# Kernel optimization log

Hardware: AMD Instinct MI355X
Metric: run time of the kernel (lower is better)

Reference implementation:

```python
import jax, jax.numpy as jnp
import numpy as np

B, L, D = 4, 816, 2048
SEP = 768            # gemma (image+text) prefix length
P_LEN = 3            # proprio tokens inside the action-expert block
N, K, H = 8, 1, 256  # heads, kv heads (GQA), head dim
G = N // K
GEMMA_MLP, ACTION_MLP = 16384, 4096
SOFTCAP = 50.0
BIG_NEG = -2.3819763e38


def rms_norm(x, scale, eps=1e-6):
    var = jnp.mean(jnp.square(x.astype(jnp.float32)), axis=-1, keepdims=True)
    normed = x * jax.lax.rsqrt(var + eps)
    return (normed * (1.0 + scale)).astype(x.dtype)


def apply_rope(x, positions, max_wavelength=10_000):
    # x: [B, T, n, H], positions: [B, T]
    head_dim = x.shape[-1]
    freq_exp = (2.0 / head_dim) * jnp.arange(head_dim // 2, dtype=jnp.float32)
    timescale = max_wavelength ** freq_exp
    radians = positions[..., None].astype(jnp.float32) / timescale[None, None, :]
    radians = radians[..., None, :]  # [B, T, 1, H/2]
    sin, cos = jnp.sin(radians), jnp.cos(radians)
    x1, x2 = jnp.split(x, 2, axis=-1)
    return jnp.concatenate([x1 * cos - x2 * sin, x2 * cos + x1 * sin], axis=-1).astype(x.dtype)


def get_qkv(xn, positions, wq, wkv):
    # wq: [N, D, H], wkv: [2, K, D, H]
    q = jnp.einsum('btd,ndh->btnh', xn, wq)
    k = jnp.einsum('bsd,kdh->bskh', xn, wkv[0])
    v = jnp.einsum('bsd,kdh->bskh', xn, wkv[1])
    q = apply_rope(q, positions) * (H ** -0.5)  # query_pre_attn_norm='rsqrt_head_dim'
    k = apply_rope(k, positions)
    return q, k, v


def geglu_ffn(x, w_gating, w_linear):
    # gemma GeGLU: w_gating [2, D, hidden], w_linear [hidden, D]
    gate = jax.nn.gelu(jnp.einsum('btd,dh->bth', x, w_gating[0]))
    act = gate * jnp.einsum('btd,dh->bth', x, w_gating[1])
    return jnp.einsum('bth,hd->btd', act, w_linear)


def setup_inputs() -> dict:
    key = jax.random.key(0)
    ks = jax.random.split(key, 16)
    s = 0.02
    x = jax.random.normal(ks[0], (B, L, D), jnp.float32)
    positions = jnp.broadcast_to(jnp.arange(L, dtype=jnp.int32), (B, L))
    # PiZero block mask: full attention within gemma prefix; proprio and action
    # blocks attend to everything before them plus themselves (mask_ar cumsum trick).
    mask_ar = np.zeros(L, dtype=np.int64)
    mask_ar[SEP] = 1
    mask_ar[SEP + P_LEN] = 1
    cm = np.cumsum(mask_ar)
    attn = cm[None, :] <= cm[:, None]  # [L_q, L_kv]
    attn_mask = jnp.asarray(np.broadcast_to(attn[None, None], (B, 1, L, L)))
    return {
        'x': x,
        'positions': positions,
        'attn_mask': attn_mask,
        'separation_idx': SEP,
        'pre_attn_scale': jnp.zeros((D,), jnp.float32),
        'pre_ffw_scale': jnp.zeros((D,), jnp.float32),
        'gq_w': jax.random.normal(ks[1], (N, D, H), jnp.float32) * s,
        'gkv_w': jax.random.normal(ks[2], (2, K, D, H), jnp.float32) * s,
        'go_w': jax.random.normal(ks[3], (N, H, D), jnp.float32) * s,
        'aq_w': jax.random.normal(ks[4], (N, D, H), jnp.float32) * s,
        'akv_w': jax.random.normal(ks[5], (2, K, D, H), jnp.float32) * s,
        'ao_w': jax.random.normal(ks[6], (N, H, D), jnp.float32) * s,
        'g_gating': jax.random.normal(ks[7], (2, D, GEMMA_MLP), jnp.float32) * s,
        'g_linear': jax.random.normal(ks[8], (GEMMA_MLP, D), jnp.float32) * s,
        'a_gating': jax.random.normal(ks[9], (2, D, ACTION_MLP), jnp.float32) * s,
        'a_linear': jax.random.normal(ks[10], (ACTION_MLP, D), jnp.float32) * s,
    }


def reference(x, positions, attn_mask, separation_idx, pre_attn_scale, pre_ffw_scale,
              gq_w, gkv_w, go_w, aq_w, akv_w, ao_w,
              g_gating, g_linear, a_gating, a_linear):
    sep = separation_idx
    xg, xa = x[:, :sep, :], x[:, sep:, :]
    # shared pre-attention RMSNorm applied to both expert streams
    ng = rms_norm(xg, pre_attn_scale)
    na = rms_norm(xa, pre_attn_scale)
    pg, pa = positions[:, :sep], positions[:, sep:]
    qg, kg, vg = get_qkv(ng, pg, gq_w, gkv_w)
    qa, ka, va = get_qkv(na, pa, aq_w, akv_w)
    # joint attention over concatenated streams
    q = jnp.concatenate([qg, qa], axis=1)   # [B, L, N, H]
    k = jnp.concatenate([kg, ka], axis=1)   # [B, L, K, H]
    v = jnp.concatenate([vg, va], axis=1)
    Bq, T = q.shape[0], q.shape[1]
    qr = q.reshape(Bq, T, K, G, H)
    logits = jnp.einsum('btkgh,bskh->bkgts', qr, k)
    logits = jnp.tanh(logits / SOFTCAP) * SOFTCAP  # attn logit softcap
    logits = jnp.where(attn_mask[:, :, None, :, :], logits, BIG_NEG)
    probs = jax.nn.softmax(logits.astype(jnp.float32), axis=-1).astype(logits.dtype)
    attn_out = jnp.einsum('bkgts,bskh->btkgh', probs, v).reshape(Bq, T, N, H)
    # per-expert output projections
    og = jnp.einsum('btnh,nhd->btd', attn_out[:, :sep], go_w)
    oa = jnp.einsum('btnh,nhd->btd', attn_out[:, sep:], ao_w)

    def post(attn_o, res, gating, lin):
        # faithful to source: final residual is mlp(norm(attn+res)) + res
        h = rms_norm(attn_o + res, pre_ffw_scale)
        return geglu_ffn(h, gating, lin) + res

    yg = post(og, xg, g_gating, g_linear)
    ya = post(oa, xa, a_gating, a_linear)
    return jnp.concatenate([yg, ya], axis=1)
```

## Files before the change

### kernel.cpp

```cpp
#include <hip/hip_runtime.h>
#include <hip/hip_bf16.h>

typedef __bf16 bfx8 __attribute__((ext_vector_type(8)));
typedef __bf16 bfx4 __attribute__((ext_vector_type(4)));
typedef float f32x4 __attribute__((ext_vector_type(4)));

#define MFMA16(a, b, c) __builtin_amdgcn_mfma_f32_16x16x32_bf16((a), (b), (c), 0, 0, 0)

__device__ __forceinline__ void gl_lds16(const __bf16* g, __bf16* l) {
  __builtin_amdgcn_global_load_lds(
      (const __attribute__((address_space(1))) unsigned int*)(const void*)g,
      (__attribute__((address_space(3))) unsigned int*)(void*)l, 16, 0, 0);
}

__device__ __forceinline__ unsigned pack_bf2(float a, float b) {
  unsigned short ua = __builtin_bit_cast(unsigned short, (__bf16)a);
  unsigned short ub = __builtin_bit_cast(unsigned short, (__bf16)b);
  return (unsigned)ua | ((unsigned)ub << 16);
}

__device__ __forceinline__ float gelu_tanh_f(float x) {
  float u = 0.7978845608028654f * (x + 0.044715f * x * x * x);
  float t;
  if (u > 10.f) t = 1.f;
  else if (u < -10.f) t = -1.f;
  else { float e = __expf(2.f * u); t = (e - 1.f) / (e + 1.f); }
  return 0.5f * x * (1.f + t);
}

__global__ __launch_bounds__(256)
void rmsnorm_kernel(const float* __restrict__ X, const float* __restrict__ X2,
                    const float* __restrict__ scale, __bf16* __restrict__ out) {
  __shared__ float wsum[4];
  const int row = blockIdx.x, tid = threadIdx.x;
  const size_t base = (size_t)row * 2048;
  f32x4 v[2];
  float ss = 0.f;
#pragma unroll
  for (int i = 0; i < 2; ++i) {
    const int idx = tid * 4 + i * 1024;
    v[i] = *(const f32x4*)(X + base + idx);
    if (X2) { f32x4 u = *(const f32x4*)(X2 + base + idx); v[i] = v[i] + u; }
#pragma unroll
    for (int j = 0; j < 4; ++j) ss += v[i][j] * v[i][j];
  }
#pragma unroll
  for (int o = 32; o > 0; o >>= 1) ss += __shfl_xor(ss, o, 64);
  if ((tid & 63) == 0) wsum[tid >> 6] = ss;
  __syncthreads();
  const float tot = wsum[0] + wsum[1] + wsum[2] + wsum[3];
  const float rs = rsqrtf(tot * (1.f / 2048.f) + 1e-6f);
#pragma unroll
  for (int i = 0; i < 2; ++i) {
    const int idx = tid * 4 + i * 1024;
    f32x4 sc = *(const f32x4*)(scale + idx);
    bfx4 ov;
#pragma unroll
    for (int j = 0; j < 4; ++j) ov[j] = (__bf16)(v[i][j] * rs * (1.f + sc[j]));
    *(bfx4*)(out + base + idx) = ov;
  }
}

__global__ __launch_bounds__(256)
void rope_bf_kernel(__bf16* __restrict__ buf, const int* __restrict__ pos,
                    int nheads, int rstride, float outscale) {
  const int row = blockIdx.x;
  const float p = (float)pos[row];
  const int total = nheads * 128;
  const size_t rbase = (size_t)row * (size_t)rstride;
  for (int idx = threadIdx.x; idx < total; idx += 256) {
    const int n = idx >> 7, i = idx & 127;
    const float ts = __expf(-(float)i * 0.071955784f);
    float sn, cs;
    __sincosf(p * ts, &sn, &cs);
    __bf16* bp = buf + rbase + n * 256 + i;
    const float x1 = (float)bp[0], x2 = (float)bp[128];
    bp[0]   = (__bf16)((x1 * cs - x2 * sn) * outscale);
    bp[128] = (__bf16)((x2 * cs + x1 * sn) * outscale);
  }
}

__global__ __launch_bounds__(256)
void rope_kernel(const float* __restrict__ in, const int* __restrict__ pos,
                 __bf16* __restrict__ outp, int nheads, float outscale) {
  const int row = blockIdx.x;
  const float p = (float)pos[row];
  const int total = nheads * 128;
  const size_t rbase = (size_t)row * (size_t)(nheads * 256);
  for (int idx = threadIdx.x; idx < total; idx += 256) {
    const int n = idx >> 7, i = idx & 127;
    const float ts = __expf(-(float)i * 0.071955784f);
    float sn, cs;
    __sincosf(p * ts, &sn, &cs);
    const float* bp = in + rbase + n * 256 + i;
    const float x1 = bp[0], x2 = bp[128];
    __bf16* ob = outp + rbase + n * 256 + i;
    ob[0]   = (__bf16)((x1 * cs - x2 * sn) * outscale);
    ob[128] = (__bf16)((x2 * cs + x1 * sn) * outscale);
  }
}

__global__ __launch_bounds__(256)
void convw_kernel(const float* __restrict__ in, __bf16* __restrict__ out,
                  int K, int headDim) {
  __shared__ __bf16 tile[64][65];
  const int tc0 = blockIdx.x * 64;
  const int tk0 = blockIdx.y * 64;
  const int tid = threadIdx.x;
  const int cchunk = tid & 15, krow = tid >> 4;
  const int c = tc0 + cchunk * 4;
  const float* colbase = in + (size_t)(c / headDim) * (size_t)K * headDim + (c % headDim);
#pragma unroll
  for (int i = 0; i < 4; ++i) {
    const int k = tk0 + krow + i * 16;
    f32x4 v = *(const f32x4*)(colbase + (size_t)k * headDim);
#pragma unroll
    for (int j = 0; j < 4; ++j) tile[cchunk * 4 + j][krow + i * 16] = (__bf16)v[j];
  }
  __syncthreads();
  const int nks = K >> 5;
#pragma unroll
  for (int s = 0; s < 2; ++s) {
    const int ch = tid + s * 256;
    const int wc = ch >> 3, wk8 = (ch & 7) * 8;
    bfx8 v;
#pragma unroll
    for (int j = 0; j < 8; ++j) v[j] = tile[wc][wk8 + j];
    const int col = tc0 + wc;
    const int kchunk = (tk0 + wk8) >> 3;
    const int cp = col >> 7, m = col & 127;
    const int ks = kchunk >> 2, lg = kchunk & 3;
    const int p = lg ^ ((m >> 1) & 3);
    *(bfx8*)(out + ((size_t)(cp * nks + ks)) * 4096 + m * 32 + p * 8) = v;
  }
}

__global__ __launch_bounds__(256, 2)
void gemm_bt2(const __bf16* __restrict__ A, const __bf16* __restrict__ Bt,
              void* __restrict__ C, void* __restrict__ C2, const void* __restrict__ Extra,
              int Mpb, int lda, int strideA, int Kd,
              int ldc, int strideC, int mbPerBatch,
              int outMode, int ldct) {
  __shared__ __align__(16) __bf16 As[8192];
  __shared__ __align__(16) __bf16 Bs[8192];
  const int tid = threadIdx.x;
  const int lane = tid & 63;
  const int wid = tid >> 6;
  const int b = blockIdx.x / mbPerBatch;
  const int row0 = (blockIdx.x % mbPerBatch) * 128;
  const int col0 = blockIdx.y * 128;
  const __bf16* Ab = A + (size_t)b * strideA;
  const size_t nks = (size_t)(Kd >> 5);
  const __bf16* Bpan0 = Bt + ((size_t)(col0 >> 7)) * nks * 4096;
  const int wm = (wid >> 1) * 64, wn = (wid & 1) * 64;
  const int qi = lane & 15, g = lane >> 4;

  const int m0 = tid >> 2, p0 = tid & 3;
  const int lg0 = p0 ^ ((m0 >> 1) & 3);
  const int m1 = m0 + 64;
  const int lg1 = p0 ^ ((m1 >> 1) & 3);
  int mr0 = row0 + m0; if (mr0 >= Mpb) mr0 = Mpb - 1;
  int mr1 = row0 + m1; if (mr1 >= Mpb) mr1 = Mpb - 1;
  const __bf16* asrc0 = Ab + (size_t)mr0 * lda + lg0 * 8;
  const __bf16* asrc1 = Ab + (size_t)mr1 * lda + lg1 * 8;

  f32x4 acc[4][4];
#pragma unroll
  for (int i = 0; i < 4; ++i)
#pragma unroll
    for (int j = 0; j < 4; ++j) acc[i][j] = f32x4{0.f, 0.f, 0.f, 0.f};

  for (int k0 = 0; k0 < Kd; k0 += 64) {
    __syncthreads();
    gl_lds16(asrc0 + k0, &As[tid * 8]);
    gl_lds16(asrc1 + k0, &As[(tid + 256) * 8]);
    gl_lds16(asrc0 + k0 + 32, &As[4096 + tid * 8]);
    gl_lds16(asrc1 + k0 + 32, &As[4096 + (tid + 256) * 8]);
    const __bf16* pb = Bpan0 + (size_t)(k0 >> 5) * 4096;
    gl_lds16(pb + tid * 8, &Bs[tid * 8]);
    gl_lds16(pb + (tid + 256) * 8, &Bs[(tid + 256) * 8]);
    gl_lds16(pb + 4096 + tid * 8, &Bs[4096 + tid * 8]);
    gl_lds16(pb + 4096 + (tid + 256) * 8, &Bs[4096 + (tid + 256) * 8]);
    __syncthreads();
#pragma unroll
    for (int ks = 0; ks < 2; ++ks) {
      bfx8 af[4], bf[4];
#pragma unroll
      for (int mi = 0; mi < 4; ++mi) {
        const int m = wm + mi * 16 + qi;
        const int sl = g ^ ((m >> 1) & 3);
        af[mi] = *(const bfx8*)(&As[ks * 4096 + m * 32 + sl * 8]);
      }
#pragma unroll
      for (int ni = 0; ni < 4; ++ni) {
        const int n = wn + ni * 16 + qi;
        const int sl = g ^ ((n >> 1) & 3);
        bf[ni] = *(const bfx8*)(&Bs[ks * 4096 + n * 32 + sl * 8]);
      }
#pragma unroll
      for (int mi = 0; mi < 4; ++mi)
#pragma unroll
        for (int ni = 0; ni < 4; ++ni)
          acc[mi][ni] = MFMA16(af[mi], bf[ni], acc[mi][ni]);
    }
  }

#pragma unroll
  for (int mi = 0; mi < 4; ++mi) {
#pragma unroll
    for (int ni = 0; ni < 4; ++ni) {
      const int col = col0 + wn + ni * 16 + qi;
      if (outMode == 5 && col >= 2304) {
        const int vcol = col - 2304;
        const int rowb = row0 + wm + mi * 16 + g * 4;
        if (rowb < Mpb) {
          bfx4 ov;
#pragma unroll
          for (int r = 0; r < 4; ++r) ov[r] = (__bf16)acc[mi][ni][r];
          *(bfx4*)((__bf16*)C2 + (size_t)b * (256 * 816) + (size_t)vcol * 816 + rowb) = ov;
        }
        continue;
      }
#pragma unroll
      for (int r = 0; r < 4; ++r) {
        const int row = row0 + wm + mi * 16 + g * 4 + r;
        if (row >= Mpb) continue;
        const float v = acc[mi][ni][r];
        if (outMode == 0) {
          ((float*)C)[(size_t)b * strideC + (size_t)row * ldc + col] = v;
        } else if (outMode == 1 || outMode == 5) {
          ((__bf16*)C)[(size_t)b * strideC + (size_t)row * ldc + col] = (__bf16)v;
        } else {
          const size_t ix = (size_t)b * strideC + (size_t)row * ldc + col;
          ((float*)C)[ix] = v + ((const float*)Extra)[ix];
        }
      }
    }
  }
  (void)ldct;
}

__global__ __launch_bounds__(256, 2)
void ffn_dual(const __bf16* __restrict__ A, const __bf16* __restrict__ Wg,
              const __bf16* __restrict__ Wa, __bf16* __restrict__ C,
              int Mpb, int lda, int strideA, int Kd,
              int ldc, int strideC, int mbPerBatch) {
  __shared__ __align__(16) __bf16 As[8192];
  __shared__ __align__(16) __bf16 Bs[8192];
  const int tid = threadIdx.x;
  const int lane = tid & 63;
  const int wid = tid >> 6;
  const int b = blockIdx.x / mbPerBatch;
  const int row0 = (blockIdx.x % mbPerBatch) * 128;
  const int col0 = blockIdx.y * 128;
  const __bf16* Ab = A + (size_t)b * strideA;
  const size_t nks = (size_t)(Kd >> 5);
  const int wm = (wid >> 1) * 64, wn = (wid & 1) * 64;
  const int qi = lane & 15, g = lane >> 4;

  const int m0 = tid >> 2, p0 = tid & 3;
  const int lg0 = p0 ^ ((m0 >> 1) & 3);
  const int m1 = m0 + 64;
  const int lg1 = p0 ^ ((m1 >> 1) & 3);
  int mr0 = row0 + m0; if (mr0 >= Mpb) mr0 = Mpb - 1;
  int mr1 = row0 + m1; if (mr1 >= Mpb) mr1 = Mpb - 1;
  const __bf16* asrc0 = Ab + (size_t)mr0 * lda + lg0 * 8;
  const __bf16* asrc1 = Ab + (size_t)mr1 * lda + lg1 * 8;

  f32x4 gval[4][4];
  f32x4 acc[4][4];

#pragma unroll
  for (int pan = 0; pan < 2; ++pan) {
    const __bf16* Bpan0 = (pan ? Wa : Wg) + ((size_t)(col0 >> 7)) * nks * 4096;
#pragma unroll
    for (int i = 0; i < 4; ++i)
#pragma unroll
      for (int j = 0; j < 4; ++j) acc[i][j] = f32x4{0.f, 0.f, 0.f, 0.f};

    for (int k0 = 0; k0 < Kd; k0 += 64) {
      __syncthreads();
      gl_lds16(asrc0 + k0, &As[tid * 8]);
      gl_lds16(asrc1 + k0, &As[(tid + 256) * 8]);
      gl_lds16(asrc0 + k0 + 32, &As[4096 + tid * 8]);
      gl_lds16(asrc1 + k0 + 32, &As[4096 + (tid + 256) * 8]);
      const __bf16* pb = Bpan0 + (size_t)(k0 >> 5) * 4096;
      gl_lds16(pb + tid * 8, &Bs[tid * 8]);
      gl_lds16(pb + (tid + 256) * 8, &Bs[tid * 8 + 2048]);
      gl_lds16(pb + 4096 + tid * 8, &Bs[4096 + tid * 8]);
      gl_lds16(pb + 4096 + (tid + 256) * 8, &Bs[4096 + tid * 8 + 2048]);
      __syncthreads();
#pragma unroll
      for (int ks = 0; ks < 2; ++ks) {
        bfx8 af[4], bf[4];
#pragma unroll
        for (int mi = 0; mi < 4; ++mi) {
          const int m = wm + mi * 16 + qi;
          const int sl = g ^ ((m >> 1) & 3);
          af[mi] = *(const bfx8*)(&As[ks * 4096 + m * 32 + sl * 8]);
        }
#pragma unroll
        for (int ni = 0; ni < 4; ++ni) {
          const int n = wn + ni * 16 + qi;
          const int sl = g ^ ((n >> 1) & 3);
          bf[ni] = *(const bfx8*)(&Bs[ks * 4096 + n * 32 + sl * 8]);
        }
#pragma unroll
        for (int mi = 0; mi < 4; ++mi)
#pragma unroll
          for (int ni = 0; ni < 4; ++ni)
            acc[mi][ni] = MFMA16(af[mi], bf[ni], acc[mi][ni]);
      }
    }

    if (pan == 0) {
#pragma unroll
      for (int i = 0; i < 4; ++i)
#pragma unroll
        for (int j = 0; j < 4; ++j)
#pragma unroll
          for (int r = 0; r < 4; ++r) gval[i][j][r] = gelu_tanh_f(acc[i][j][r]);
    }
  }

#pragma unroll
  for (int mi = 0; mi < 4; ++mi) {
#pragma unroll
    for (int ni = 0; ni < 4; ++ni) {
      const int col = col0 + wn + ni * 16 + qi;
#pragma unroll
      for (int r = 0; r < 4; ++r) {
        const int row = row0 + wm + mi * 16 + g * 4 + r;
        if (row >= Mpb) continue;
        C[(size_t)b * strideC + (size_t)row * ldc + col] =
            (__bf16)(gval[mi][ni][r] * acc[mi][ni][r]);
      }
    }
  }
}


__global__ __launch_bounds__(256, 2)
void gemm_kernel(const __bf16* __restrict__ A, const float* __restrict__ Bw,
                 void* __restrict__ C, const void* __restrict__ Extra,
                 int Mpb, int lda, int strideA,
                 int ldb, int headDim, int Kd,
                 int ldc, int strideC, int mbPerBatch,
                 int outMode, int ldct) {
  __shared__ __align__(16) __bf16 As[128 * 32];
  __shared__ __align__(16) __bf16 Bs[128 * 32];
  const int tid = threadIdx.x;
  const int lane = tid & 63;
  const int wid = tid >> 6;
  const int b = blockIdx.x / mbPerBatch;
  const int row0 = (blockIdx.x % mbPerBatch) * 128;
  const int col0 = blockIdx.y * 128;
  const __bf16* Ab = A + (size_t)b * strideA;
  const float* Bb = (headDim > 0)
      ? (Bw + (size_t)(col0 / headDim) * (size_t)Kd * headDim + (col0 % headDim))
      : (Bw + col0);
  const int wm = (wid >> 1) * 64, wn = (wid & 1) * 64;
  const int qi = lane & 15, g = lane >> 4;

  f32x4 acc[4][4];
#pragma unroll
  for (int i = 0; i < 4; ++i)
#pragma unroll
    for (int j = 0; j < 4; ++j) acc[i][j] = f32x4{0.f, 0.f, 0.f, 0.f};

  const int am = tid >> 2, ap = tid & 3;
  const int bn = tid >> 2, bc = tid & 3;

  for (int k0 = 0; k0 < Kd; k0 += 32) {
    __syncthreads();
#pragma unroll
    for (int s = 0; s < 2; ++s) {
      const int m = am + s * 64;
      int mr = row0 + m;
      if (mr >= Mpb) mr = Mpb - 1;
      const int lg = ap ^ ((m >> 1) & 3);
      bfx8 v = *(const bfx8*)(Ab + (size_t)mr * lda + k0 + lg * 8);
      *(bfx8*)(&As[m * 32 + ap * 8]) = v;
    }
#pragma unroll
    for (int s = 0; s < 2; ++s) {
      const int n = bn + s * 64;
      const float* bp = Bb + (size_t)(k0 + bc * 8) * ldb + n;
      bfx8 v;
#pragma unroll
      for (int i = 0; i < 8; ++i) v[i] = (__bf16)bp[(size_t)i * ldb];
      const int p = bc ^ ((n >> 1) & 3);
      *(bfx8*)(&Bs[n * 32 + p * 8]) = v;
    }
    __syncthreads();
    bfx8 af[4], bf[4];
#pragma unroll
    for (int mi = 0; mi < 4; ++mi) {
      const int m = wm + mi * 16 + qi;
      const int sl = g ^ ((m >> 1) & 3);
      af[mi] = *(const bfx8*)(&As[m * 32 + sl * 8]);
    }
#pragma unroll
    for (int ni = 0; ni < 4; ++ni) {
      const int n = wn + ni * 16 + qi;
      const int sl = g ^ ((n >> 1) & 3);
      bf[ni] = *(const bfx8*)(&Bs[n * 32 + sl * 8]);
    }
#pragma unroll
    for (int mi = 0; mi < 4; ++mi)
#pragma unroll
      for (int ni = 0; ni < 4; ++ni)
        acc[mi][ni] = MFMA16(af[mi], bf[ni], acc[mi][ni]);
  }

#pragma unroll
  for (int mi = 0; mi < 4; ++mi) {
#pragma unroll
    for (int ni = 0; ni < 4; ++ni) {
      const int col = col0 + wn + ni * 16 + qi;
#pragma unroll
      for (int r = 0; r < 4; ++r) {
        const int row = row0 + wm + mi * 16 + g * 4 + r;
        if (row >= Mpb) continue;
        const float v = acc[mi][ni][r];
        if (outMode == 0) {
          ((float*)C)[(size_t)b * strideC + (size_t)row * ldc + col] = v;
        } else if (outMode == 1) {
          ((__bf16*)C)[(size_t)b * strideC + (size_t)row * ldc + col] = (__bf16)v;
        } else if (outMode == 2) {
          const size_t ix = (size_t)b * strideC + (size_t)row * ldc + col;
          ((float*)C)[ix] = v + ((const float*)Extra)[ix];
        } else if (outMode == 3) {
          ((__bf16*)C)[(size_t)b * strideC + (size_t)col * ldct + row] = (__bf16)v;
        } else {
          const size_t ix = (size_t)b * strideC + (size_t)row * ldc + col;
          const float gt = (float)((const __bf16*)Extra)[ix];
          ((__bf16*)C)[ix] = (__bf16)(gelu_tanh_f(gt) * v);
        }
      }
    }
  }
}

__global__ __launch_bounds__(256, 2)
void attn_kernel(const __bf16* __restrict__ qp, const __bf16* __restrict__ kp0,
                 const __bf16* __restrict__ vt, __bf16* __restrict__ ao,
                 int qstride, int kstride) {
  __shared__ __align__(16) __bf16 Ps[4][1024];
  __shared__ float denw[4][16];
  const int tid = threadIdx.x, lane = tid & 63, wid = tid >> 6;
  const int qt = blockIdx.x, hn = blockIdx.y, b = blockIdx.z;
  const int q0 = qt * 64;
  const int qi = lane & 15, g = lane >> 4;

  int qrow = q0 + wid * 16 + qi;
  if (qrow > 815) qrow = 815;
  const int cmq = (qrow >= 768) + (qrow >= 771);
  const __bf16* qrp = qp + (size_t)(b * 816 + qrow) * qstride + hn * 256 + g * 8;
  bfx8 qf[8];
#pragma unroll
  for (int kf = 0; kf < 8; ++kf) qf[kf] = *(const bfx8*)(qrp + kf * 32);

  f32x4 oacc[16];
#pragma unroll
  for (int i = 0; i < 16; ++i) oacc[i] = f32x4{0.f, 0.f, 0.f, 0.f};
  float den = 0.f;

  const int ntiles = (q0 + 63 < 768) ? 12 : 13;
  for (int t = 0; t < ntiles; ++t) {
    const int kv0 = t * 64;
#pragma unroll
    for (int mi = 0; mi < 4; ++mi) {
      f32x4 sac = f32x4{0.f, 0.f, 0.f, 0.f};
      int srow = kv0 + mi * 16 + qi;
      if (srow > 815) srow = 815;
      const __bf16* kp = kp0 + (size_t)(b * 816 + srow) * kstride + g * 8;
#pragma unroll
      for (int kf = 0; kf < 8; ++kf) {
        bfx8 a = *(const bfx8*)(kp + kf * 32);
        sac = MFMA16(a, qf[kf], sac);
      }
      float pv[4];
#pragma unroll
      for (int r = 0; r < 4; ++r) {
        const int s = kv0 + mi * 16 + g * 4 + r;
        const float l = sac[r];
        const float e2 = __expf(l * 0.04f);
        const float capped = 50.f * (e2 - 1.f) / (e2 + 1.f);
        const int cms = (s >= 768) + (s >= 771);
        const bool ok = (s < 816) && (cms <= cmq);
        const float p = ok ? __expf(capped) : 0.f;
        den += p;
        pv[r] = p;
      }
      const unsigned lo = pack_bf2(pv[0], pv[1]);
      const unsigned hi = pack_bf2(pv[2], pv[3]);
      const int slot = 2 * mi + (g >> 1);
      const int phys = slot ^ (qi & 7);
      char* pb = (char*)&Ps[wid][0] + qi * 128 + phys * 16 + (g & 1) * 8;
      *(unsigned*)(pb) = lo;
      *(unsigned*)(pb + 4) = hi;
    }
    asm volatile("s_waitcnt lgkmcnt(0)" ::: "memory");
    bfx8 pa[2];
#pragma unroll
    for (int k2 = 0; k2 < 2; ++k2) {
      const int sl = (k2 * 4 + g) ^ (qi & 7);
      pa[k2] = *(const bfx8*)((const char*)&Ps[wid][0] + qi * 128 + sl * 16);
    }
#pragma unroll
    for (int hf = 0; hf < 16; ++hf) {
      const int h = hf * 16 + qi;
#pragma unroll
      for (int k2 = 0; k2 < 2; ++k2) {
        int s0 = kv0 + k2 * 32 + g * 8;
        if (s0 > 808) s0 = 808;
        bfx8 vb = *(const bfx8*)(vt + ((size_t)(b * 256 + h)) * 816 + s0);
        oacc[hf] = MFMA16(pa[k2], vb, oacc[hf]);
      }
    }
    asm volatile("s_waitcnt lgkmcnt(0)" ::: "memory");
  }

  den += __shfl_xor(den, 16, 64);
  den += __shfl_xor(den, 32, 64);
  if (lane < 16) denw[wid][qi] = den;
  asm volatile("s_waitcnt lgkmcnt(0)" ::: "memory");
#pragma unroll
  for (int r = 0; r < 4; ++r) {
    const int qg = q0 + wid * 16 + g * 4 + r;
    if (qg >= 816) continue;
    const float di = 1.f / denw[wid][g * 4 + r];
#pragma unroll
    for (int hf = 0; hf < 16; ++hf) {
      ao[((size_t)(b * 816 + qg)) * 2048 + hn * 256 + hf * 16 + qi] =
          (__bf16)(oacc[hf][r] * di);
    }
  }
}

extern "C" void kernel_launch(void* const* d_in, const int* in_sizes, int n_in,
                              void* d_out, int out_size, void* d_ws, size_t ws_size,
                              hipStream_t stream) {
  (void)in_sizes; (void)n_in; (void)out_size;
  const float* x      = (const float*)d_in[0];
  const int*   pos    = (const int*)d_in[1];
  const float* s_attn = (const float*)d_in[4];
  const float* s_ffw  = (const float*)d_in[5];
  const float* gq     = (const float*)d_in[6];
  const float* gkv    = (const float*)d_in[7];
  const float* go     = (const float*)d_in[8];
  const float* aq     = (const float*)d_in[9];
  const float* akv    = (const float*)d_in[10];
  const float* aow    = (const float*)d_in[11];
  const float* gg     = (const float*)d_in[12];
  const float* gl     = (const float*)d_in[13];
  const float* ag     = (const float*)d_in[14];
  const float* al     = (const float*)d_in[15];
  float* outp = (float*)d_out;
  char* ws = (char*)d_ws;
  dim3 blk(256);

  const size_t NEED_BATCH = 577437696u;
  const size_t NEED_FAST  = 423297024u;

  if (ws_size >= NEED_FAST) {
    const bool batched = (ws_size >= NEED_BATCH);
    __bf16* wQKVg = (__bf16*)(ws + 0);
    __bf16* wQKVa = (__bf16*)(ws + 10485760);
    __bf16* goT = (__bf16*)(ws + 20971520);
    __bf16* aoT = (__bf16*)(ws + 29360128);
    __bf16* ggT = (__bf16*)(ws + 37748736);
    __bf16* glT = (__bf16*)(ws + 171966464);
    __bf16* agT = (__bf16*)(ws + 239075328);
    __bf16* alT = (__bf16*)(ws + 272629760);
    __bf16* xn   = (__bf16*)(ws + 289406976);
    __bf16* qkb  = (__bf16*)(ws + 302776320);
    __bf16* vt   = (__bf16*)(ws + 317816832);
    __bf16* aob  = (__bf16*)(ws + 319488000);
    float*  ob   = (float*)(ws + 332857344);
    __bf16* hb   = (__bf16*)(ws + 359596032);
    __bf16* gate  = (__bf16*)(ws + 372965376);
    __bf16* act   = (__bf16*)(ws + 398131200);
    __bf16* act4  = (__bf16*)(ws + 473628672);
    __bf16* actA4 = (__bf16*)(ws + 575864832);

    convw_kernel<<<dim3(32, 32), blk, 0, stream>>>(gq, wQKVg, 2048, 256);
    convw_kernel<<<dim3(4, 32), blk, 0, stream>>>(gkv, wQKVg + 16 * 64 * 4096, 2048, 256);
    convw_kernel<<<dim3(4, 32), blk, 0, stream>>>(gkv + 2048 * 256, wQKVg + 18 * 64 * 4096, 2048, 256);
    convw_kernel<<<dim3(32, 32), blk, 0, stream>>>(aq, wQKVa, 2048, 256);
    convw_kernel<<<dim3(4, 32), blk, 0, stream>>>(akv, wQKVa + 16 * 64 * 4096, 2048, 256);
    convw_kernel<<<dim3(4, 32), blk, 0, stream>>>(akv + 2048 * 256, wQKVa + 18 * 64 * 4096, 2048, 256);
    convw_kernel<<<dim3(32, 32), blk, 0, stream>>>(go, goT, 2048, 2048);
    convw_kernel<<<dim3(32, 32), blk, 0, stream>>>(aow, aoT, 2048, 2048);
    convw_kernel<<<dim3(256, 32), blk, 0, stream>>>(gg, ggT, 2048, 16384);
    convw_kernel<<<dim3(256, 32), blk, 0, stream>>>(gg + (size_t)2048 * 16384, ggT + (size_t)16384 * 2048, 2048, 16384);
    convw_kernel<<<dim3(32, 256), blk, 0, stream>>>(gl, glT, 16384, 2048);
    convw_kernel<<<dim3(64, 32), blk, 0, stream>>>(ag, agT, 2048, 4096);
    convw_kernel<<<dim3(64, 32), blk, 0, stream>>>(ag + (size_t)2048 * 4096, agT + (size_t)4096 * 2048, 2048, 4096);
    convw_kernel<<<dim3(32, 64), blk, 0, stream>>>(al, alT, 4096, 2048);

    rmsnorm_kernel<<<3264, blk, 0, stream>>>(x, nullptr, s_attn, xn);

    gemm_bt2<<<dim3(24, 20), blk, 0, stream>>>(xn, wQKVg, qkb, vt, nullptr,
        768, 2048, 816 * 2048, 2048, 2304, 816 * 2304, 6, 5, 0);
    gemm_bt2<<<dim3(4, 20), blk, 0, stream>>>(xn + 768 * 2048, wQKVa, qkb + 768 * 2304, vt + 768, nullptr,
        48, 2048, 816 * 2048, 2048, 2304, 816 * 2304, 1, 5, 0);

    rope_bf_kernel<<<3264, blk, 0, stream>>>(qkb, pos, 8, 2304, 0.0625f);
    rope_bf_kernel<<<3264, blk, 0, stream>>>(qkb + 2048, pos, 1, 2304, 1.0f);

    attn_kernel<<<dim3(13, 8, 4), blk, 0, stream>>>(qkb, qkb + 2048, vt, aob, 2304, 2304);

    gemm_bt2<<<dim3(24, 16), blk, 0, stream>>>(aob, goT, ob, nullptr, nullptr,
        768, 2048, 816 * 2048, 2048, 2048, 816 * 2048, 6, 0, 0);
    gemm_bt2<<<dim3(4, 16), blk, 0, stream>>>(aob + 768 * 2048, aoT, ob + 768 * 2048, nullptr, nullptr,
        48, 2048, 816 * 2048, 2048, 2048, 816 * 2048, 1, 0, 0);

    rmsnorm_kernel<<<3264, blk, 0, stream>>>(ob, x, s_ffw, hb);

    if (batched) {
      ffn_dual<<<dim3(24, 128), blk, 0, stream>>>(hb, ggT, ggT + (size_t)16384 * 2048, act4,
          768, 2048, 816 * 2048, 2048, 16384, 768 * 16384, 6);
      gemm_bt2<<<dim3(24, 16), blk, 0, stream>>>(act4, glT, outp, nullptr, x,
          768, 16384, 768 * 16384, 16384, 2048, 816 * 2048, 6, 2, 0);
      ffn_dual<<<dim3(4, 32), blk, 0, stream>>>(hb + 768 * 2048, agT, agT + (size_t)4096 * 2048, actA4,
          48, 2048, 816 * 2048, 2048, 4096, 48 * 4096, 1);
      gemm_bt2<<<dim3(4, 16), blk, 0, stream>>>(actA4, alT, outp + 768 * 2048, nullptr, x + 768 * 2048,
          48, 4096, 48 * 4096, 4096, 2048, 816 * 2048, 1, 2, 0);
    } else {
      for (int bb = 0; bb < 4; ++bb) {
        const __bf16* hg = hb + (size_t)bb * 816 * 2048;
        float* og = outp + (size_t)bb * 816 * 2048;
        const float* xg = x + (size_t)bb * 816 * 2048;
        ffn_dual<<<dim3(6, 128), blk, 0, stream>>>(hg, ggT, ggT + (size_t)16384 * 2048, act,
            768, 2048, 0, 2048, 16384, 0, 6);
        gemm_bt2<<<dim3(6, 16), blk, 0, stream>>>(act, glT, og, nullptr, xg,
            768, 16384, 0, 16384, 2048, 0, 6, 2, 0);
        const __bf16* ha = hg + 768 * 2048;
        ffn_dual<<<dim3(1, 32), blk, 0, stream>>>(ha, agT, agT + (size_t)4096 * 2048, gate,
            48, 2048, 0, 2048, 4096, 0, 1);
        gemm_bt2<<<dim3(1, 16), blk, 0, stream>>>(gate, alT, og + 768 * 2048, nullptr, xg + 768 * 2048,
            48, 4096, 0, 4096, 2048, 0, 1, 2, 0);
      }
    }
    return;
  }

  if (ws_size < 164000000u) return;
  __bf16* xn   = (__bf16*)(ws + 0);
  float*  qf   = (float*)(ws + 13369344);
  __bf16* qbb  = (__bf16*)(ws + 40108032);
  float*  kf   = (float*)(ws + 53477376);
  __bf16* kbb  = (__bf16*)(ws + 56819712);
  __bf16* vt   = (__bf16*)(ws + 58490880);
  __bf16* aob  = (__bf16*)(ws + 60162048);
  float*  ob   = (float*)(ws + 73531392);
  __bf16* hb   = (__bf16*)(ws + 100270080);
  __bf16* gate = (__bf16*)(ws + 113639424);
  __bf16* act  = (__bf16*)(ws + 138805248);

  rmsnorm_kernel<<<3264, blk, 0, stream>>>(x, nullptr, s_attn, xn);
  gemm_kernel<<<dim3(24, 16), blk, 0, stream>>>(xn, gq, qf, nullptr,
      768, 2048, 816 * 2048, 256, 256, 2048, 2048, 816 * 2048, 6, 0, 0);
  gemm_kernel<<<dim3(4, 16), blk, 0, stream>>>(xn + 768 * 2048, aq, qf + 768 * 2048, nullptr,
      48, 2048, 816 * 2048, 256, 256, 2048, 2048, 816 * 2048, 1, 0, 0);
  gemm_kernel<<<dim3(24, 2), blk, 0, stream>>>(xn, gkv, kf, nullptr,
      768, 2048, 816 * 2048, 256, 256, 2048, 256, 816 * 256, 6, 0, 0);
  gemm_kernel<<<dim3(4, 2), blk, 0, stream>>>(xn + 768 * 2048, akv, kf + 768 * 256, nullptr,
      48, 2048, 816 * 2048, 256, 256, 2048, 256, 816 * 256, 1, 0, 0);
  gemm_kernel<<<dim3(24, 2), blk, 0, stream>>>(xn, gkv + 2048 * 256, vt, nullptr,
      768, 2048, 816 * 2048, 256, 256, 2048, 0, 256 * 816, 6, 3, 816);
  gemm_kernel<<<dim3(4, 2), blk, 0, stream>>>(xn + 768 * 2048, akv + 2048 * 256, vt + 768, nullptr,
      48, 2048, 816 * 2048, 256, 256, 2048, 0, 256 * 816, 1, 3, 816);
  rope_kernel<<<3264, blk, 0, stream>>>(qf, pos, qbb, 8, 0.0625f);
  rope_kernel<<<3264, blk, 0, stream>>>(kf, pos, kbb, 1, 1.0f);
  attn_kernel<<<dim3(13, 8, 4), blk, 0, stream>>>(qbb, kbb, vt, aob, 2048, 256);
  gemm_kernel<<<dim3(24, 16), blk, 0, stream>>>(aob, go, ob, nullptr,
      768, 2048, 816 * 2048, 2048, 0, 2048, 2048, 816 * 2048, 6, 0, 0);
  gemm_kernel<<<dim3(4, 16), blk, 0, stream>>>(aob + 768 * 2048, aow, ob + 768 * 2048, nullptr,
      48, 2048, 816 * 2048, 2048, 0, 2048, 2048, 816 * 2048, 1, 0, 0);
  rmsnorm_kernel<<<3264, blk, 0, stream>>>(ob, x, s_ffw, hb);
  for (int bb = 0; bb < 4; ++bb) {
    const __bf16* hg = hb + (size_t)bb * 816 * 2048;
    float* og = outp + (size_t)bb * 816 * 2048;
    const float* xg = x + (size_t)bb * 816 * 2048;
    gemm_kernel<<<dim3(6, 128), blk, 0, stream>>>(hg, gg, gate, nullptr,
        768, 2048, 0, 16384, 0, 2048, 16384, 0, 6, 1, 0);
    gemm_kernel<<<dim3(6, 128), blk, 0, stream>>>(hg, gg + 2048 * 16384, act, gate,
        768, 2048, 0, 16384, 0, 2048, 16384, 0, 6, 4, 0);
    gemm_kernel<<<dim3(6, 16), blk, 0, stream>>>(act, gl, og, xg,
        768, 16384, 0, 2048, 0, 16384, 2048, 0, 6, 2, 0);
    const __bf16* ha = hg + 768 * 2048;
    gemm_kernel<<<dim3(1, 32), blk, 0, stream>>>(ha, ag, gate, nullptr,
        48, 2048, 0, 4096, 0, 2048, 4096, 0, 1, 1, 0);
    gemm_kernel<<<dim3(1, 32), blk, 0, stream>>>(ha, ag + 2048 * 4096, act, gate,
        48, 2048, 0, 4096, 0, 2048, 4096, 0, 1, 4, 0);
    gemm_kernel<<<dim3(1, 16), blk, 0, stream>>>(act, al, og + 768 * 2048, xg + 768 * 2048,
        48, 4096, 0, 2048, 0, 4096, 2048, 0, 1, 2, 0);
  }
}
```

Measured before the change: 1.565 ms.

## Double-buffer LDS tiles in gemm_bt2 and ffn_dual to overlap loads with MFMA

Converts the single-buffered K loop in the two main bf16 GEMM kernels into a two-stage pipeline. Tiles t and t+1 are prefetched into alternating LDS buffers via global_load_lds, with explicit vmcnt waits and barriers between stages. The goal is to hide global memory latency behind MFMA compute instead of stalling at a barrier on every K step. LDS use per block doubles to 64KB, which may limit the two-blocks-per-CU occupancy. Correctness also depends on the hand-counted vmcnt(8) matching the eight loads issued per stage.

```diff
diff --git a/kernel.cpp b/kernel.cpp
--- a/kernel.cpp
+++ b/kernel.cpp
@@ -141,8 +141,8 @@
               int Mpb, int lda, int strideA, int Kd,
               int ldc, int strideC, int mbPerBatch,
               int outMode, int ldct) {
-  __shared__ __align__(16) __bf16 As[8192];
-  __shared__ __align__(16) __bf16 Bs[8192];
+  __shared__ __align__(16) __bf16 As[2][8192];
+  __shared__ __align__(16) __bf16 Bs[2][8192];
   const int tid = threadIdx.x;
   const int lane = tid & 63;
   const int wid = tid >> 6;
@@ -163,6 +163,20 @@
   int mr1 = row0 + m1; if (mr1 >= Mpb) mr1 = Mpb - 1;
   const __bf16* asrc0 = Ab + (size_t)mr0 * lda + lg0 * 8;
   const __bf16* asrc1 = Ab + (size_t)mr1 * lda + lg1 * 8;
+  const int nt = Kd >> 6;
+
+  auto stage = [&](int t, int bufi) {
+    const int k0 = t * 64;
+    gl_lds16(asrc0 + k0, &As[bufi][tid * 8]);
+    gl_lds16(asrc1 + k0, &As[bufi][(tid + 256) * 8]);
+    gl_lds16(asrc0 + k0 + 32, &As[bufi][4096 + tid * 8]);
+    gl_lds16(asrc1 + k0 + 32, &As[bufi][4096 + (tid + 256) * 8]);
+    const __bf16* pb = Bpan0 + (size_t)(k0 >> 5) * 4096;
+    gl_lds16(pb + tid * 8, &Bs[bufi][tid * 8]);
+    gl_lds16(pb + (tid + 256) * 8, &Bs[bufi][(tid + 256) * 8]);
+    gl_lds16(pb + 4096 + tid * 8, &Bs[bufi][4096 + tid * 8]);
+    gl_lds16(pb + 4096 + (tid + 256) * 8, &Bs[bufi][4096 + (tid + 256) * 8]);
+  };
 
   f32x4 acc[4][4];
 #pragma unroll
@@ -170,18 +184,15 @@
 #pragma unroll
     for (int j = 0; j < 4; ++j) acc[i][j] = f32x4{0.f, 0.f, 0.f, 0.f};
 
-  for (int k0 = 0; k0 < Kd; k0 += 64) {
-    __syncthreads();
-    gl_lds16(asrc0 + k0, &As[tid * 8]);
-    gl_lds16(asrc1 + k0, &As[(tid + 256) * 8]);
-    gl_lds16(asrc0 + k0 + 32, &As[4096 + tid * 8]);
-    gl_lds16(asrc1 + k0 + 32, &As[4096 + (tid + 256) * 8]);
-    const __bf16* pb = Bpan0 + (size_t)(k0 >> 5) * 4096;
-    gl_lds16(pb + tid * 8, &Bs[tid * 8]);
-    gl_lds16(pb + (tid + 256) * 8, &Bs[(tid + 256) * 8]);
-    gl_lds16(pb + 4096 + tid * 8, &Bs[4096 + tid * 8]);
-    gl_lds16(pb + 4096 + (tid + 256) * 8, &Bs[4096 + (tid + 256) * 8]);
-    __syncthreads();
+  stage(0, 0);
+  if (nt > 1) stage(1, 1);
+
+  for (int t = 0; t < nt; ++t) {
+    const int cur = t & 1;
+    if (t + 1 < nt) asm volatile("s_waitcnt vmcnt(8)" ::: "memory");
+    else            asm volatile("s_waitcnt vmcnt(0)" ::: "memory");
+    __builtin_amdgcn_s_barrier();
+    asm volatile("" ::: "memory");
 #pragma unroll
     for (int ks = 0; ks < 2; ++ks) {
       bfx8 af[4], bf[4];
@@ -189,13 +200,13 @@
       for (int mi = 0; mi < 4; ++mi) {
         const int m = wm + mi * 16 + qi;
         const int sl = g ^ ((m >> 1) & 3);
-        af[mi] = *(const bfx8*)(&As[ks * 4096 + m * 32 + sl * 8]);
+        af[mi] = *(const bfx8*)(&As[cur][ks * 4096 + m * 32 + sl * 8]);
       }
 #pragma unroll
       for (int ni = 0; ni < 4; ++ni) {
         const int n = wn + ni * 16 + qi;
         const int sl = g ^ ((n >> 1) & 3);
-        bf[ni] = *(const bfx8*)(&Bs[ks * 4096 + n * 32 + sl * 8]);
+        bf[ni] = *(const bfx8*)(&Bs[cur][ks * 4096 + n * 32 + sl * 8]);
       }
 #pragma unroll
       for (int mi = 0; mi < 4; ++mi)
@@ -203,6 +214,10 @@
         for (int ni = 0; ni < 4; ++ni)
           acc[mi][ni] = MFMA16(af[mi], bf[ni], acc[mi][ni]);
     }
+    asm volatile("s_waitcnt lgkmcnt(0)" ::: "memory");
+    __builtin_amdgcn_s_barrier();
+    asm volatile("" ::: "memory");
+    if (t + 2 < nt) stage(t + 2, cur);
   }
 
 #pragma unroll
@@ -245,8 +260,8 @@
               const __bf16* __restrict__ Wa, __bf16* __restrict__ C,
               int Mpb, int lda, int strideA, int Kd,
               int ldc, int strideC, int mbPerBatch) {
-  __shared__ __align__(16) __bf16 As[8192];
-  __shared__ __align__(16) __bf16 Bs[8192];
+  __shared__ __align__(16) __bf16 As[2][8192];
+  __shared__ __align__(16) __bf16 Bs[2][8192];
   const int tid = threadIdx.x;
   const int lane = tid & 63;
   const int wid = tid >> 6;
@@ -266,6 +281,7 @@
   int mr1 = row0 + m1; if (mr1 >= Mpb) mr1 = Mpb - 1;
   const __bf16* asrc0 = Ab + (size_t)mr0 * lda + lg0 * 8;
   const __bf16* asrc1 = Ab + (size_t)mr1 * lda + lg1 * 8;
+  const int nt = Kd >> 6;
 
   f32x4 gval[4][4];
   f32x4 acc[4][4];
@@ -273,23 +289,34 @@
 #pragma unroll
   for (int pan = 0; pan < 2; ++pan) {
     const __bf16* Bpan0 = (pan ? Wa : Wg) + ((size_t)(col0 >> 7)) * nks * 4096;
+
+    auto stage = [&](int t, int bufi) {
+      const int k0 = t * 64;
+      gl_lds16(asrc0 + k0, &As[bufi][tid * 8]);
+      gl_lds16(asrc1 + k0, &As[bufi][(tid + 256) * 8]);
+      gl_lds16(asrc0 + k0 + 32, &As[bufi][4096 + tid * 8]);
+      gl_lds16(asrc1 + k0 + 32, &As[bufi][4096 + (tid + 256) * 8]);
+      const __bf16* pb = Bpan0 + (size_t)(k0 >> 5) * 4096;
+      gl_lds16(pb + tid * 8, &Bs[bufi][tid * 8]);
+      gl_lds16(pb + (tid + 256) * 8, &Bs[bufi][(tid + 256) * 8]);
+      gl_lds16(pb + 4096 + tid * 8, &Bs[bufi][4096 + tid * 8]);
+      gl_lds16(pb + 4096 + (tid + 256) * 8, &Bs[bufi][4096 + (tid + 256) * 8]);
+    };
+
 #pragma unroll
     for (int i = 0; i < 4; ++i)
 #pragma unroll
       for (int j = 0; j < 4; ++j) acc[i][j] = f32x4{0.f, 0.f, 0.f, 0.f};
 
-    for (int k0 = 0; k0 < Kd; k0 += 64) {
-      __syncthreads();
-      gl_lds16(asrc0 + k0, &As[tid * 8]);
-      gl_lds16(asrc1 + k0, &As[(tid + 256) * 8]);
-      gl_lds16(asrc0 + k0 + 32, &As[4096 + tid * 8]);
-      gl_lds16(asrc1 + k0 + 32, &As[4096 + (tid + 256) * 8]);
-      const __bf16* pb = Bpan0 + (size_t)(k0 >> 5) * 4096;
-      gl_lds16(pb + tid * 8, &Bs[tid * 8]);
-      gl_lds16(pb + (tid + 256) * 8, &Bs[tid * 8 + 2048]);
-      gl_lds16(pb + 4096 + tid * 8, &Bs[4096 + tid * 8]);
-      gl_lds16(pb + 4096 + (tid + 256) * 8, &Bs[4096 + tid * 8 + 2048]);
-      __syncthreads();
+    stage(0, 0);
+    if (nt > 1) stage(1, 1);
+
+    for (int t = 0; t < nt; ++t) {
+      const int cur = t & 1;
+      if (t + 1 < nt) asm volatile("s_waitcnt vmcnt(8)" ::: "memory");
+      else            asm volatile("s_waitcnt vmcnt(0)" ::: "memory");
+      __builtin_amdgcn_s_barrier();
+      asm volatile("" ::: "memory");
 #pragma unroll
       for (int ks = 0; ks < 2; ++ks) {
         bfx8 af[4], bf[4];
@@ -297,13 +324,13 @@
         for (int mi = 0; mi < 4; ++mi) {
           const int m = wm + mi * 16 + qi;
           const int sl = g ^ ((m >> 1) & 3);
-          af[mi] = *(const bfx8*)(&As[ks * 4096 + m * 32 + sl * 8]);
+          af[mi] = *(const bfx8*)(&As[cur][ks * 4096 + m * 32 + sl * 8]);
         }
 #pragma unroll
         for (int ni = 0; ni < 4; ++ni) {
           const int n = wn + ni * 16 + qi;
           const int sl = g ^ ((n >> 1) & 3);
-          bf[ni] = *(const bfx8*)(&Bs[ks * 4096 + n * 32 + sl * 8]);
+          bf[ni] = *(const bfx8*)(&Bs[cur][ks * 4096 + n * 32 + sl * 8]);
         }
 #pragma unroll
         for (int mi = 0; mi < 4; ++mi)
@@ -311,6 +338,10 @@
           for (int ni = 0; ni < 4; ++ni)
             acc[mi][ni] = MFMA16(af[mi], bf[ni], acc[mi][ni]);
       }
+      asm volatile("s_waitcnt lgkmcnt(0)" ::: "memory");
+      __builtin_amdgcn_s_barrier();
+      asm volatile("" ::: "memory");
+      if (t + 2 < nt) stage(t + 2, cur);
     }
 
     if (pan == 0) {
@@ -338,7 +369,6 @@
     }
   }
 }
-
 
 __global__ __launch_bounds__(256, 2)
 void gemm_kernel(const __bf16* __restrict__ A, const float* __restrict__ Bw,
```

New measurement: 1.549 ms. Within noise of the previous version (-1.0%).
